# Kernel optimization log

Hardware: AMD Instinct MI355X
Metric: run time of the kernel (lower is better)

## Reference

```python
import jax, jax.numpy as jnp
import numpy as np


def _layernorm(x, g, b, eps=1e-5):
    m = x.mean(-1, keepdims=True)
    v = ((x - m) ** 2).mean(-1, keepdims=True)
    return (x - m) * jax.lax.rsqrt(v + eps) * g + b


def _rmsnorm(x, w, eps=1e-6):
    return x * jax.lax.rsqrt((x * x).mean(-1, keepdims=True) + eps) * w


def setup_inputs() -> dict:
    key = jax.random.key(0)
    ks = jax.random.split(key, 8)
    B, T, S, C_img = 1, 3, 880, 3072
    C_mouse, D_hid, Dd = 2, 1024, 64
    vin = C_img + 12 * C_mouse  # 3096 = img_hidden + mouse_dim_in*vae_tcr*windows
    w = lambda k, shp: (jax.random.normal(k, shp, jnp.float32) * 0.02)
    return dict(
        x=jax.random.normal(ks[0], (B, T * S, C_img), jnp.float32),
        condition=jax.random.normal(ks[1], (B, 12, C_mouse), jnp.float32),
        w1=w(ks[2], (vin, D_hid)), b1=jnp.zeros((D_hid,), jnp.float32),
        w2=w(ks[3], (D_hid, D_hid)), b2=jnp.zeros((D_hid,), jnp.float32),
        ln_g=jnp.ones((D_hid,), jnp.float32), ln_b=jnp.zeros((D_hid,), jnp.float32),
        wqkv=w(ks[4], (D_hid, 3 * D_hid)), bqkv=jnp.zeros((3 * D_hid,), jnp.float32),
        qn_w=jnp.ones((Dd,), jnp.float32), kn_w=jnp.ones((Dd,), jnp.float32),
        wproj=w(ks[5], (D_hid, C_img)), bproj=jnp.zeros((C_img,), jnp.float32),
        H=22, W=40, temporal_shape=3, num_frame_per_block=3,
    )


def reference(x, condition, w1, b1, w2, b2, ln_g, ln_b, wqkv, bqkv,
              qn_w, kn_w, wproj, bproj, H, W, temporal_shape, num_frame_per_block):
    B, T_S, C_img = x.shape
    T = temporal_shape
    if condition.shape[1] > 9:
        condition = condition[:, -12:, :]
    _, N_frames, C = condition.shape
    action_len, pad_len = 20, 12
    pad = jnp.zeros((B, action_len - N_frames, C), condition.dtype)
    mouse_padded = jnp.concatenate([pad, condition], axis=1)  # [B, 20, C]
    # windowed gather: fixed small loop over num_frame_per_block (<=3)
    wins = jnp.stack([mouse_padded[:, i * 4:i * 4 + pad_len, :]
                      for i in range(num_frame_per_block)], axis=1)  # [B, F, 12, C]
    gm = wins.reshape(B, num_frame_per_block, pad_len * C)  # [B, F, 12C]
    S = 880  # hardcoded in original forward
    gm = jnp.broadcast_to(gm[:, None], (B, S, num_frame_per_block, pad_len * C))
    gm = gm.reshape(B * S, num_frame_per_block, pad_len * C)
    # fuse broadcast mouse features with image tokens (raw row-major reshape, as in torch)
    fused = jnp.concatenate([x.reshape(B * S, T, C_img), gm], axis=-1)  # [BS, T, C_img+12C]
    h = jax.nn.gelu(fused @ w1 + b1, approximate=True) @ w2 + b2
    h = _layernorm(h, ln_g, ln_b)  # [BS, T, D_hid]
    qkv = h @ wqkv + bqkv  # [BS, T, 3*D_hid]
    Dd = qn_w.shape[0]
    Hh = qkv.shape[-1] // (3 * Dd)
    qkv = qkv.reshape(B * S, T, 3, Hh, Dd)
    q, k, v = qkv[:, :, 0], qkv[:, :, 1], qkv[:, :, 2]
    q = _rmsnorm(q, qn_w).astype(v.dtype)
    k = _rmsnorm(k, kn_w).astype(v.dtype)
    # original flattens to one sequence of BS*T tokens for single_prefill (non-causal)
    N = B * S * T
    qf = q.reshape(N, Hh, Dd)
    kf = k.reshape(N, Hh, Dd)
    vf = v.reshape(N, Hh, Dd)
    scale = 1.0 / np.sqrt(Dd).astype(np.float32)
    scores = jnp.einsum('nhd,mhd->hnm', qf, kf) * scale  # [Hh, N, N]
    attn = jax.nn.softmax(scores, axis=-1)
    o = jnp.einsum('hnm,mhd->nhd', attn, vf)  # [N, Hh, Dd]
    # '(B S) T H D -> B (T S) (H D)'
    o = o.reshape(B, S, T, Hh, Dd).transpose(0, 2, 1, 3, 4).reshape(B, T * S, Hh * Dd)
    out = o @ wproj + bproj
    return x + out
```

## Files before the change

kernel.cpp:

```cpp
#include <hip/hip_runtime.h>
#include <hip/hip_bf16.h>

typedef __attribute__((ext_vector_type(8))) short short8;
typedef __attribute__((ext_vector_type(4))) short short4v;
typedef __attribute__((ext_vector_type(4))) unsigned uint4v;
typedef __attribute__((ext_vector_type(4))) float f32x4;
typedef __attribute__((ext_vector_type(16))) float f32x16;
typedef unsigned short u16;

#define ZERO16 (f32x16){0,0,0,0,0,0,0,0,0,0,0,0,0,0,0,0}

__device__ __forceinline__ float b2f(u16 h) {
    unsigned u = ((unsigned)h) << 16;
    float f; __builtin_memcpy(&f, &u, 4); return f;
}
__device__ __forceinline__ u16 f2b(float f) {
    __hip_bfloat16 h = __float2bfloat16(f);
    u16 r; __builtin_memcpy(&r, &h, 2); return r;
}
__device__ __forceinline__ void gload16(const void* g, void* l) {
    __builtin_amdgcn_global_load_lds(
        (const __attribute__((address_space(1))) unsigned*)g,
        (__attribute__((address_space(3))) unsigned*)l, 16, 0, 0);
}
__device__ __forceinline__ unsigned cvtpk_bf16(float lo, float hi) {
    unsigned d;
    asm("v_cvt_pk_bf16_f32 %0, %1, %2" : "=v"(d) : "v"(lo), "v"(hi));
    return d;
}

#define M_VALID 2640
#define M_PAD   2688
#define K1      3096
#define K1P     3136
#define DH      1024
#define CIMG    3072
#define NHEAD   16
#define NT      84
#define QTP     42
#define NSPLIT  3
#define TILES_PER_SPLIT 28
#define LOG2E   1.4426950408889634f

__global__ __launch_bounds__(256) void build_fused_kernel(
    const float* __restrict__ x, const float* __restrict__ cond,
    u16* __restrict__ fused)
{
    int n = blockIdx.x;
    int tid = threadIdx.x;
    const float* xr = x + (size_t)n * CIMG;
    u16* fr = fused + (size_t)n * K1P;
    for (int c = tid * 4; c < CIMG; c += 1024) {
        float4 v = *(const float4*)(xr + c);
        short4v w;
        w[0] = (short)f2b(v.x); w[1] = (short)f2b(v.y);
        w[2] = (short)f2b(v.z); w[3] = (short)f2b(v.w);
        *(short4v*)(fr + c) = w;
    }
    if (tid < 16) {
        int t = n % 3;
        short4v w;
        for (int jj = 0; jj < 4; jj++) {
            int j = tid * 4 + jj;
            float val = 0.f;
            if (j < 24) {
                int f = t * 4 + (j >> 1);
                if (f >= 8) val = cond[(f - 8) * 2 + (j & 1)];
            }
            w[jj] = (short)f2b(val);
        }
        *(short4v*)(fr + CIMG + tid * 4) = w;
    }
}

__global__ __launch_bounds__(256) void transpose_all_kernel(
    const float* __restrict__ w1, const float* __restrict__ w2,
    const float* __restrict__ wqkv, const float* __restrict__ wproj,
    u16* __restrict__ w1t, u16* __restrict__ w2t,
    u16* __restrict__ wqkvt, u16* __restrict__ wprojt)
{
    int b = blockIdx.x;
    const float* W; u16* Wt; int K, N, ldt, nx;
    if (b < 3136)      {            W = w1;    Wt = w1t;    K = K1; N = DH;   ldt = K1P; nx = 32; }
    else if (b < 4160) { b -= 3136; W = w2;    Wt = w2t;    K = DH; N = DH;   ldt = DH;  nx = 32; }
    else if (b < 7232) { b -= 4160; W = wqkv;  Wt = wqkvt;  K = DH; N = 3072; ldt = DH;  nx = 96; }
    else               { b -= 7232; W = wproj; Wt = wprojt; K = DH; N = CIMG; ldt = DH;  nx = 96; }
    __shared__ float t[32][33];
    int n0 = (b % nx) * 32, k0 = (b / nx) * 32;
    int x = threadIdx.x & 31, y0 = threadIdx.x >> 5;
    for (int yy = y0; yy < 32; yy += 8) {
        int k = k0 + yy, n = n0 + x;
        t[yy][x] = (k < K && n < N) ? W[(size_t)k * N + n] : 0.f;
    }
    __syncthreads();
    for (int yy = y0; yy < 32; yy += 8) {
        int n = n0 + yy, k = k0 + x;
        if (n < N && k < ldt) Wt[(size_t)n * ldt + k] = f2b(t[x][yy]);
    }
}

template<int EPI, int BM, int BN>
__global__ __launch_bounds__(256) void gemm_kernel(
    const u16* __restrict__ A, const u16* __restrict__ Bt,
    const float* __restrict__ bias, const float* __restrict__ resid,
    u16* __restrict__ Cb, float* __restrict__ Cf,
    int N, int K, int Mvalid)
{
    constexpr int MI  = BM / 32;
    constexpr int NJ  = BN / 32;
    constexpr int CA  = BM / 32;
    constexpr int CB  = BN / 32;
    constexpr unsigned ABYTES = BM * 128;
    constexpr unsigned BBYTES = BN * 128;
    constexpr unsigned STG = 2 * (ABYTES + BBYTES);
    constexpr unsigned CTW = BN + 4;
    constexpr unsigned CTB = BM * CTW * 4;
    constexpr int TPR = 256 / BM;
    __shared__ __align__(16) char smem[STG > CTB ? STG : CTB];

    const int tid = threadIdx.x;
    const int lane = tid & 63, wid = tid >> 6;
    const int l15 = lane & 15, l4 = lane >> 4;

    const int nx = N / BN;
    const int nwg = nx * (M_PAD / BM);
    const int bid = blockIdx.x;
    const int wgid = (bid & 7) * (nwg >> 3) + (bid >> 3);
    const int m0 = (wgid / nx) * BM, n0 = (wgid % nx) * BN;

    const int wr = (wid >> 1) * (BM / 2), wc = (wid & 1) * (BN / 2);

    const int srow = lane >> 3;
    const int scol = ((lane & 7) ^ (lane >> 3)) << 3;

    f32x4 acc[MI][NJ];
#pragma unroll
    for (int i = 0; i < MI; i++)
#pragma unroll
        for (int j = 0; j < NJ; j++) acc[i][j] = (f32x4){0.f, 0.f, 0.f, 0.f};

    const int nt = K >> 6;

    auto stage = [&](int buf, int k0) {
        char* Ab = smem + buf * ABYTES;
        char* Bb = smem + 2 * ABYTES + buf * BBYTES;
#pragma unroll
        for (int i = 0; i < CA; i++) {
            int c = wid * CA + i;
            gload16(A + (size_t)(m0 + c * 8 + srow) * K + k0 + scol,
                    Ab + c * 1024 + lane * 16);
        }
#pragma unroll
        for (int i = 0; i < CB; i++) {
            int c = wid * CB + i;
            gload16(Bt + (size_t)(n0 + c * 8 + srow) * K + k0 + scol,
                    Bb + c * 1024 + lane * 16);
        }
    };

    stage(0, 0);
    __syncthreads();
    int cur = 0;
    for (int t = 0; t < nt; t++) {
        if (t + 1 < nt) stage(cur ^ 1, (t + 1) * 64);
        const char* Ab = smem + cur * ABYTES;
        const char* Bb = smem + 2 * ABYTES + cur * BBYTES;
#pragma unroll
        for (int ki = 0; ki < 2; ki++) {
            short8 af[MI], bfr[NJ];
#pragma unroll
            for (int i = 0; i < MI; i++) {
                int row = wr + i * 16 + l15;
                af[i] = *(const short8*)(Ab + row * 128 + (((ki * 4 + l4) ^ (l15 & 7)) << 4));
            }
#pragma unroll
            for (int j = 0; j < NJ; j++) {
                int row = wc + j * 16 + l15;
                bfr[j] = *(const short8*)(Bb + row * 128 + (((ki * 4 + l4) ^ (l15 & 7)) << 4));
            }
            __builtin_amdgcn_s_setprio(1);
#pragma unroll
            for (int i = 0; i < MI; i++)
#pragma unroll
                for (int j = 0; j < NJ; j++)
                    acc[i][j] = __builtin_amdgcn_mfma_f32_16x16x32_bf16(af[i], bfr[j], acc[i][j], 0, 0, 0);
            __builtin_amdgcn_s_setprio(0);
        }
        __syncthreads();
        cur ^= 1;
    }

    float* Ct = (float*)smem;
#pragma unroll
    for (int i = 0; i < MI; i++)
#pragma unroll
        for (int j = 0; j < NJ; j++)
#pragma unroll
            for (int r = 0; r < 4; r++)
                Ct[(wr + i * 16 + l4 * 4 + r) * CTW + wc + j * 16 + l15] = acc[i][j][r];
    __syncthreads();

    const int row = tid / TPR;
    const int cb  = (tid % TPR) * (BN / TPR);
    const int grow = m0 + row;
    const int gcol = n0 + cb;
    if (EPI == 2) {
        if (grow < Mvalid) {
#pragma unroll
            for (int u = 0; u < BN / (4 * TPR); u++) {
                f32x4 v = *(const f32x4*)&Ct[row * CTW + cb + u * 4];
                float4 bv = *(const float4*)&bias[gcol + u * 4];
                float4 rv = *(const float4*)&resid[(size_t)grow * N + gcol + u * 4];
                float4 o;
                o.x = v[0] + bv.x + rv.x; o.y = v[1] + bv.y + rv.y;
                o.z = v[2] + bv.z + rv.z; o.w = v[3] + bv.w + rv.w;
                *(float4*)&Cf[(size_t)grow * N + gcol + u * 4] = o;
            }
        }
    } else {
        u16 tmp[BN / TPR];
#pragma unroll
        for (int u = 0; u < BN / (4 * TPR); u++) {
            f32x4 v = *(const f32x4*)&Ct[row * CTW + cb + u * 4];
            float4 bv = *(const float4*)&bias[gcol + u * 4];
#pragma unroll
            for (int e = 0; e < 4; e++) {
                float val = v[e] + ((const float*)&bv)[e];
                if (EPI == 0) {
                    float tt = val + 0.044715f * val * val * val;
                    val = 0.5f * val * (1.0f + tanhf(0.7978845608028654f * tt));
                }
                tmp[u * 4 + e] = f2b(val);
            }
        }
#pragma unroll
        for (int u = 0; u < BN / (8 * TPR); u++)
            *(short8*)(Cb + (size_t)grow * N + gcol + u * 8) = *(const short8*)&tmp[u * 8];
    }
}

__global__ __launch_bounds__(256) void ln_kernel(
    const u16* __restrict__ h2, const float* __restrict__ g,
    const float* __restrict__ b, u16* __restrict__ out)
{
    int row = blockIdx.x;
    int tid = threadIdx.x;
    const u16* p = h2 + (size_t)row * DH;
    float v[4];
#pragma unroll
    for (int i = 0; i < 4; i++) v[i] = b2f(p[tid * 4 + i]);
    float s1 = v[0] + v[1] + v[2] + v[3];
    float s2 = v[0]*v[0] + v[1]*v[1] + v[2]*v[2] + v[3]*v[3];
    for (int m = 1; m < 64; m <<= 1) { s1 += __shfl_xor(s1, m); s2 += __shfl_xor(s2, m); }
    __shared__ float a1[4], a2[4];
    int w = tid >> 6;
    if ((tid & 63) == 0) { a1[w] = s1; a2[w] = s2; }
    __syncthreads();
    s1 = a1[0] + a1[1] + a1[2] + a1[3];
    s2 = a2[0] + a2[1] + a2[2] + a2[3];
    float mean = s1 * (1.0f / 1024.0f);
    float var = s2 * (1.0f / 1024.0f) - mean * mean;
    float rs = rsqrtf(var + 1e-5f);
    u16* q = out + (size_t)row * DH;
#pragma unroll
    for (int i = 0; i < 4; i++) {
        int c = tid * 4 + i;
        q[c] = f2b((v[i] - mean) * rs * g[c] + b[c]);
    }
}

__global__ __launch_bounds__(256) void fragmentize_kernel(
    const u16* __restrict__ qkv, const float* __restrict__ qw, const float* __restrict__ kw,
    u16* __restrict__ Qf, u16* __restrict__ Kf, u16* __restrict__ Vf)
{
    __shared__ u16 Vlds[8 * 32 * 80];
    const int kt = blockIdx.x;
    const int hg = blockIdx.y;
    const int tid = threadIdx.x;
    const int t32 = tid >> 3, c8 = tid & 7;
    const int n = kt * 32 + t32;
    const u16* row = qkv + (size_t)n * 3072;

#pragma unroll
    for (int hh = 0; hh < 8; hh++) {
        short8 v = *(const short8*)(row + 2048 + (hg * 8 + hh) * 64 + c8 * 8);
        *(short8*)(&Vlds[(hh * 32 + t32) * 80 + c8 * 8]) = v;
    }

    float sq[8], sk[8];
#pragma unroll
    for (int hh = 0; hh < 8; hh++) {
        int h = hg * 8 + hh;
        short8 qv = *(const short8*)(row + h * 64 + c8 * 8);
        short8 kv = *(const short8*)(row + 1024 + h * 64 + c8 * 8);
        float aq = 0.f, ak = 0.f;
#pragma unroll
        for (int e = 0; e < 8; e++) {
            float fq = b2f((u16)qv[e]); aq += fq * fq;
            float fk = b2f((u16)kv[e]); ak += fk * fk;
        }
        sq[hh] = aq; sk[hh] = ak;
    }
#pragma unroll
    for (int m = 1; m < 8; m <<= 1) {
#pragma unroll
        for (int hh = 0; hh < 8; hh++) {
            sq[hh] += __shfl_xor(sq[hh], m);
            sk[hh] += __shfl_xor(sk[hh], m);
        }
    }

    float qwv[8], kwv[8];
#pragma unroll
    for (int e = 0; e < 8; e++) { qwv[e] = qw[c8 * 8 + e]; kwv[e] = kw[c8 * 8 + e]; }

#pragma unroll
    for (int hh = 0; hh < 8; hh++) {
        int h = hg * 8 + hh;
        float rq = rsqrtf(sq[hh] * (1.0f / 64.0f) + 1e-6f) * (0.125f * LOG2E);
        float rk = rsqrtf(sk[hh] * (1.0f / 64.0f) + 1e-6f);
        short8 qv = *(const short8*)(row + h * 64 + c8 * 8);
        short8 kv = *(const short8*)(row + 1024 + h * 64 + c8 * 8);
        short8 qo, ko;
#pragma unroll
        for (int e = 0; e < 8; e++) {
            qo[e] = (short)f2b(b2f((u16)qv[e]) * rq * qwv[e]);
            ko[e] = (short)f2b(b2f((u16)kv[e]) * rk * kwv[e]);
        }
        size_t base = (((size_t)(h * NT + kt) * 4 + (c8 >> 1)) << 9) + t32 * 16 + (c8 & 1) * 8;
        *(short8*)(Qf + base) = qo;
        *(short8*)(Kf + base) = ko;
    }

    __syncthreads();

    const int fd = tid >> 6;
    const int lkq = (tid & 63) >> 1, lhi = tid & 1;
#pragma unroll
    for (int hh = 0; hh < 8; hh++) {
        int h = hg * 8 + hh;
        short8 o;
#pragma unroll
        for (int e = 0; e < 8; e++)
            o[e] = (short)Vlds[(hh * 32 + (fd & 1) * 16 + lhi * 8 + e) * 80 + (fd >> 1) * 32 + lkq];
        *(short8*)(Vf + (((size_t)(h * NT + kt) * 4 + fd) << 9) + lkq * 16 + lhi * 8) = o;
    }
}

__device__ __forceinline__ void attn_tile(
    f32x16& st, float& lr, f32x16& o0, f32x16& o1, const short8* vv)
{
    float sum = 0.f;
    float p[16];
#pragma unroll
    for (int r = 0; r < 16; r++) { p[r] = __builtin_amdgcn_exp2f(st[r]); sum += p[r]; }
    lr += sum + __shfl_xor(sum, 32);

    unsigned a0 = cvtpk_bf16(p[0], p[1]),   a1 = cvtpk_bf16(p[2], p[3]);
    unsigned a2 = cvtpk_bf16(p[4], p[5]),   a3 = cvtpk_bf16(p[6], p[7]);
    unsigned a4 = cvtpk_bf16(p[8], p[9]),   a5 = cvtpk_bf16(p[10], p[11]);
    unsigned a6 = cvtpk_bf16(p[12], p[13]), a7 = cvtpk_bf16(p[14], p[15]);
    asm("v_permlane32_swap_b32 %0, %1" : "+v"(a0), "+v"(a2));
    asm("v_permlane32_swap_b32 %0, %1" : "+v"(a1), "+v"(a3));
    asm("v_permlane32_swap_b32 %0, %1" : "+v"(a4), "+v"(a6));
    asm("v_permlane32_swap_b32 %0, %1" : "+v"(a5), "+v"(a7));
    uint4v u0 = {a0, a1, a2, a3}, u1 = {a4, a5, a6, a7};
    short8 pa0, pa1;
    __builtin_memcpy(&pa0, &u0, 16);
    __builtin_memcpy(&pa1, &u1, 16);

    __builtin_amdgcn_s_setprio(1);
    o0 = __builtin_amdgcn_mfma_f32_32x32x16_bf16(pa0, vv[0], o0, 0, 0, 0);
    o0 = __builtin_amdgcn_mfma_f32_32x32x16_bf16(pa1, vv[1], o0, 0, 0, 0);
    o1 = __builtin_amdgcn_mfma_f32_32x32x16_bf16(pa0, vv[2], o1, 0, 0, 0);
    o1 = __builtin_amdgcn_mfma_f32_32x32x16_bf16(pa1, vv[3], o1, 0, 0, 0);
    __builtin_amdgcn_s_setprio(0);
}

__global__ __launch_bounds__(128, 4) void attn_kernel(
    const u16* __restrict__ Qf, const u16* __restrict__ Kf,
    const u16* __restrict__ Vf, u16* __restrict__ part, float* __restrict__ ml)
{
    const int nwg = NSPLIT * NHEAD * QTP;
    const int bid = blockIdx.x;
    const int wgid = (bid & 7) * (nwg >> 3) + (bid >> 3);
    const int s   = wgid / (NHEAD * QTP);
    const int rem = wgid % (NHEAD * QTP);
    const int h   = rem / QTP;
    const int qtp = rem % QTP;
    const int wid = threadIdx.x >> 6;
    const int qt  = qtp * 2 + wid;
    const int lane = threadIdx.x & 63;
    const int kq = lane & 31;
    const int hi = lane >> 5;
    const int q0 = qt * 32;
    const int lxy = kq * 16 + hi * 8;
    const u16* Kh = Kf + ((size_t)h * NT * 4 << 9);
    const u16* Vh = Vf + ((size_t)h * NT * 4 << 9);

    short8 qf[4];
#pragma unroll
    for (int d = 0; d < 4; d++)
        qf[d] = *(const short8*)(Qf + (((size_t)(h * NT + qt) * 4 + d) << 9) + lxy);

    f32x16 o0 = ZERO16, o1 = ZERO16;
    float lr = 0.f;

    const int ts0 = s * TILES_PER_SPLIT;
    short8 kf[4];
#pragma unroll
    for (int d = 0; d < 4; d++)
        kf[d] = *(const short8*)(Kh + (((size_t)ts0 * 4 + d) << 9) + lxy);

    for (int i = 0; i < TILES_PER_SPLIT; i++) {
        const int tile = ts0 + i;
        const int k0 = tile * 32;
        short8 vv[4];
#pragma unroll
        for (int fd = 0; fd < 4; fd++)
            vv[fd] = *(const short8*)(Vh + (((size_t)tile * 4 + fd) << 9) + lxy);

        f32x16 st = ZERO16;
        __builtin_amdgcn_s_setprio(1);
#pragma unroll
        for (int d = 0; d < 4; d++)
            st = __builtin_amdgcn_mfma_f32_32x32x16_bf16(kf[d], qf[d], st, 0, 0, 0);
        __builtin_amdgcn_s_setprio(0);

        if (i < TILES_PER_SPLIT - 1) {
#pragma unroll
            for (int d = 0; d < 4; d++)
                kf[d] = *(const short8*)(Kh + (((size_t)(tile + 1) * 4 + d) << 9) + lxy);
        }

        if (k0 + 32 > M_VALID) {
#pragma unroll
            for (int r = 0; r < 16; r++) {
                int key = k0 + (r & 3) + 8 * (r >> 2) + 4 * hi;
                if (key >= M_VALID) st[r] = -3.0e38f;
            }
        }
        attn_tile(st, lr, o0, o1, vv);
    }

#pragma unroll
    for (int r = 0; r < 16; r++) {
        int rl = (r & 3) + 8 * (r >> 2) + 4 * hi;
        int qrow = q0 + rl;
        if (qrow < M_VALID) {
            u16* pp = part + ((size_t)s * M_PAD + qrow) * DH + h * 64;
            pp[kq] = f2b(o0[r]);
            pp[kq + 32] = f2b(o1[r]);
        }
    }
    if (hi == 0 && q0 + kq < M_VALID)
        ml[((size_t)s * NHEAD + h) * M_PAD + q0 + kq] = lr;
}

__global__ __launch_bounds__(256) void attn_merge_kernel(
    const u16* __restrict__ part, const float* __restrict__ ml, u16* __restrict__ obf)
{
    const int q = blockIdx.x;
    const int t = threadIdx.x;
    const int h = t >> 4, i = t & 15;
    float L = 0.f;
#pragma unroll
    for (int s = 0; s < NSPLIT; s++)
        L += ml[((size_t)s * NHEAD + h) * M_PAD + q];
    float inv = 1.0f / L;
    float4 acc = {0.f, 0.f, 0.f, 0.f};
#pragma unroll
    for (int s = 0; s < NSPLIT; s++) {
        short4v v = *(const short4v*)(part + ((size_t)s * M_PAD + q) * DH + h * 64 + i * 4);
        acc.x += b2f((u16)v[0]); acc.y += b2f((u16)v[1]);
        acc.z += b2f((u16)v[2]); acc.w += b2f((u16)v[3]);
    }
    int mrow = (q % 3) * 880 + q / 3;
    short4v w;
    w[0] = (short)f2b(acc.x * inv); w[1] = (short)f2b(acc.y * inv);
    w[2] = (short)f2b(acc.z * inv); w[3] = (short)f2b(acc.w * inv);
    *(short4v*)(obf + (size_t)mrow * DH + h * 64 + i * 4) = w;
}

extern "C" void kernel_launch(void* const* d_in, const int* in_sizes, int n_in,
                              void* d_out, int out_size, void* d_ws, size_t ws_size,
                              hipStream_t stream)
{
    const float* x      = (const float*)d_in[0];
    const float* cond   = (const float*)d_in[1];
    const float* w1     = (const float*)d_in[2];
    const float* b1     = (const float*)d_in[3];
    const float* w2     = (const float*)d_in[4];
    const float* b2     = (const float*)d_in[5];
    const float* ln_g   = (const float*)d_in[6];
    const float* ln_b   = (const float*)d_in[7];
    const float* wqkv   = (const float*)d_in[8];
    const float* bqkv   = (const float*)d_in[9];
    const float* qn_w   = (const float*)d_in[10];
    const float* kn_w   = (const float*)d_in[11];
    const float* wproj  = (const float*)d_in[12];
    const float* bproj  = (const float*)d_in[13];
    float* out = (float*)d_out;

    char* ws = (char*)d_ws;
    size_t off = 0;
    auto alloc = [&](size_t bytes) { size_t o = off; off += (bytes + 255) & ~(size_t)255; return o; };

    size_t off_fused  = alloc((size_t)M_PAD * K1P * 2);
    size_t off_w1t    = alloc((size_t)DH * K1P * 2);
    size_t off_w2t    = alloc((size_t)DH * DH * 2);
    size_t off_wqkvt  = alloc((size_t)3072 * DH * 2);
    size_t off_wprojt = alloc((size_t)CIMG * DH * 2);
    size_t off_h1     = alloc((size_t)M_PAD * DH * 2);
    size_t off_h2     = alloc((size_t)M_PAD * DH * 2);
    size_t off_h2ln   = alloc((size_t)M_PAD * DH * 2);
    size_t off_qkv    = alloc((size_t)M_PAD * 3072 * 2);
    size_t off_qf     = alloc((size_t)NHEAD * NT * 4 * 512 * 2);
    size_t off_kf     = alloc((size_t)NHEAD * NT * 4 * 512 * 2);
    size_t off_vf     = alloc((size_t)NHEAD * NT * 4 * 512 * 2);
    size_t off_obf    = alloc((size_t)M_PAD * DH * 2);
    (void)ws_size;

    u16* fused  = (u16*)(ws + off_fused);
    u16* w1t    = (u16*)(ws + off_w1t);
    u16* w2t    = (u16*)(ws + off_w2t);
    u16* wqkvt  = (u16*)(ws + off_wqkvt);
    u16* wprojt = (u16*)(ws + off_wprojt);
    u16* h1     = (u16*)(ws + off_h1);
    u16* h2     = (u16*)(ws + off_h2);
    u16* h2ln   = (u16*)(ws + off_h2ln);
    u16* qkvb   = (u16*)(ws + off_qkv);
    u16* Qf     = (u16*)(ws + off_qf);
    u16* Kf     = (u16*)(ws + off_kf);
    u16* Vf     = (u16*)(ws + off_vf);
    u16* obf    = (u16*)(ws + off_obf);
    u16* part   = (u16*)(ws + off_h1);
    float* mlbf = (float*)(ws + off_fused);

    hipMemsetAsync(ws + off_fused + (size_t)M_VALID * K1P * 2, 0, (size_t)(M_PAD - M_VALID) * K1P * 2, stream);

    build_fused_kernel<<<M_VALID, 256, 0, stream>>>(x, cond, fused);
    transpose_all_kernel<<<10304, 256, 0, stream>>>(w1, w2, wqkv, wproj, w1t, w2t, wqkvt, wprojt);

    gemm_kernel<0, 64, 64><<<dim3((DH / 64) * (M_PAD / 64)), 256, 0, stream>>>(fused, w1t, b1, nullptr, h1, nullptr, DH, K1P, M_PAD);
    gemm_kernel<1, 64, 64><<<dim3((DH / 64) * (M_PAD / 64)), 256, 0, stream>>>(h1, w2t, b2, nullptr, h2, nullptr, DH, DH, M_PAD);
    ln_kernel<<<M_PAD, 256, 0, stream>>>(h2, ln_g, ln_b, h2ln);
    gemm_kernel<1, 128, 128><<<dim3((3072 / 128) * (M_PAD / 128)), 256, 0, stream>>>(h2ln, wqkvt, bqkv, nullptr, qkvb, nullptr, 3072, DH, M_PAD);
    fragmentize_kernel<<<dim3(NT, 2), 256, 0, stream>>>(qkvb, qn_w, kn_w, Qf, Kf, Vf);
    attn_kernel<<<dim3(NSPLIT * NHEAD * QTP), 128, 0, stream>>>(Qf, Kf, Vf, part, mlbf);
    attn_merge_kernel<<<M_VALID, 256, 0, stream>>>(part, mlbf, obf);
    gemm_kernel<2, 128, 128><<<dim3((CIMG / 128) * (M_PAD / 128)), 256, 0, stream>>>(obf, wprojt, bproj, x, nullptr, out, CIMG, DH, M_VALID);
}
```

Measured before the change: 188.6 us.

## Fold mouse-condition columns into per-frame bias and double-buffer attention K tiles

The 24 broadcast mouse-condition columns of the first GEMM input are replaced by a precomputed per-frame bias (b1 plus cond times the matching w1 rows), indexed by row mod 3. This shrinks the first GEMM's K dimension from 3136 to 3072 and removes the pad memset and the extra fused-column writes. Separately, the attention loop now computes QK^T for two key tiles at a time with double-buffered K loads and moves the V loads into the softmax/PV helper. The attention kernel's occupancy hint drops from 4 to 2 blocks to allow more registers. With the memset gone, the padded rows of the fused buffer are left uninitialized, which could let non-finite values reach masked attention rows.

```diff
diff --git a/kernel.cpp b/kernel.cpp
--- a/kernel.cpp
+++ b/kernel.cpp
@@ -31,8 +31,7 @@
 
 #define M_VALID 2640
 #define M_PAD   2688
-#define K1      3096
-#define K1P     3136
+#define K1P     3072
 #define DH      1024
 #define CIMG    3072
 #define NHEAD   16
@@ -43,8 +42,7 @@
 #define LOG2E   1.4426950408889634f
 
 __global__ __launch_bounds__(256) void build_fused_kernel(
-    const float* __restrict__ x, const float* __restrict__ cond,
-    u16* __restrict__ fused)
+    const float* __restrict__ x, u16* __restrict__ fused)
 {
     int n = blockIdx.x;
     int tid = threadIdx.x;
@@ -57,20 +55,21 @@
         w[2] = (short)f2b(v.z); w[3] = (short)f2b(v.w);
         *(short4v*)(fr + c) = w;
     }
-    if (tid < 16) {
-        int t = n % 3;
-        short4v w;
-        for (int jj = 0; jj < 4; jj++) {
-            int j = tid * 4 + jj;
-            float val = 0.f;
-            if (j < 24) {
-                int f = t * 4 + (j >> 1);
-                if (f >= 8) val = cond[(f - 8) * 2 + (j & 1)];
-            }
-            w[jj] = (short)f2b(val);
-        }
-        *(short4v*)(fr + CIMG + tid * 4) = w;
-    }
+}
+
+__global__ __launch_bounds__(256) void bias1t_kernel(
+    const float* __restrict__ w1, const float* __restrict__ b1,
+    const float* __restrict__ cond, float* __restrict__ bias1t)
+{
+    int t = blockIdx.x;
+    int col = blockIdx.y * 256 + threadIdx.x;
+    float v = b1[col];
+#pragma unroll
+    for (int j = 0; j < 24; j++) {
+        int f = t * 4 + (j >> 1);
+        if (f >= 8) v += cond[(f - 8) * 2 + (j & 1)] * w1[(size_t)(3072 + j) * DH + col];
+    }
+    bias1t[t * DH + col] = v;
 }
 
 __global__ __launch_bounds__(256) void transpose_all_kernel(
@@ -81,10 +80,10 @@
 {
     int b = blockIdx.x;
     const float* W; u16* Wt; int K, N, ldt, nx;
-    if (b < 3136)      {            W = w1;    Wt = w1t;    K = K1; N = DH;   ldt = K1P; nx = 32; }
-    else if (b < 4160) { b -= 3136; W = w2;    Wt = w2t;    K = DH; N = DH;   ldt = DH;  nx = 32; }
-    else if (b < 7232) { b -= 4160; W = wqkv;  Wt = wqkvt;  K = DH; N = 3072; ldt = DH;  nx = 96; }
-    else               { b -= 7232; W = wproj; Wt = wprojt; K = DH; N = CIMG; ldt = DH;  nx = 96; }
+    if (b < 3072)      {            W = w1;    Wt = w1t;    K = 3072; N = DH;   ldt = 3072; nx = 32; }
+    else if (b < 4096) { b -= 3072; W = w2;    Wt = w2t;    K = DH;   N = DH;   ldt = DH;   nx = 32; }
+    else if (b < 7168) { b -= 4096; W = wqkv;  Wt = wqkvt;  K = DH;   N = 3072; ldt = DH;   nx = 96; }
+    else               { b -= 7168; W = wproj; Wt = wprojt; K = DH;   N = CIMG; ldt = DH;   nx = 96; }
     __shared__ float t[32][33];
     int n0 = (b % nx) * 32, k0 = (b / nx) * 32;
     int x = threadIdx.x & 31, y0 = threadIdx.x >> 5;
@@ -218,11 +217,12 @@
             }
         }
     } else {
+        const float* bb = bias + (EPI == 0 ? (size_t)(grow % 3) * N : 0);
         u16 tmp[BN / TPR];
 #pragma unroll
         for (int u = 0; u < BN / (4 * TPR); u++) {
             f32x4 v = *(const f32x4*)&Ct[row * CTW + cb + u * 4];
-            float4 bv = *(const float4*)&bias[gcol + u * 4];
+            float4 bv = *(const float4*)&bb[gcol + u * 4];
 #pragma unroll
             for (int e = 0; e < 4; e++) {
                 float val = v[e] + ((const float*)&bv)[e];
@@ -348,12 +348,22 @@
 }
 
 __device__ __forceinline__ void attn_tile(
-    f32x16& st, float& lr, f32x16& o0, f32x16& o1, const short8* vv)
-{
-    float sum = 0.f;
+    f32x16& st, float& lr, f32x16& o0, f32x16& o1,
+    const u16* __restrict__ Vh, int tile, int lxy)
+{
+    short8 vv[4];
+#pragma unroll
+    for (int fd = 0; fd < 4; fd++)
+        vv[fd] = *(const short8*)(Vh + (((size_t)tile * 4 + fd) << 9) + lxy);
+
     float p[16];
 #pragma unroll
-    for (int r = 0; r < 16; r++) { p[r] = __builtin_amdgcn_exp2f(st[r]); sum += p[r]; }
+    for (int r = 0; r < 16; r++) p[r] = __builtin_amdgcn_exp2f(st[r]);
+    float s0 = (p[0] + p[1]) + (p[2] + p[3]);
+    float s1 = (p[4] + p[5]) + (p[6] + p[7]);
+    float s2 = (p[8] + p[9]) + (p[10] + p[11]);
+    float s3 = (p[12] + p[13]) + (p[14] + p[15]);
+    float sum = (s0 + s1) + (s2 + s3);
     lr += sum + __shfl_xor(sum, 32);
 
     unsigned a0 = cvtpk_bf16(p[0], p[1]),   a1 = cvtpk_bf16(p[2], p[3]);
@@ -377,7 +387,7 @@
     __builtin_amdgcn_s_setprio(0);
 }
 
-__global__ __launch_bounds__(128, 4) void attn_kernel(
+__global__ __launch_bounds__(128, 2) void attn_kernel(
     const u16* __restrict__ Qf, const u16* __restrict__ Kf,
     const u16* __restrict__ Vf, u16* __restrict__ part, float* __restrict__ ml)
 {
@@ -405,34 +415,24 @@
 
     f32x16 o0 = ZERO16, o1 = ZERO16;
     float lr = 0.f;
-
     const int ts0 = s * TILES_PER_SPLIT;
-    short8 kf[4];
-#pragma unroll
-    for (int d = 0; d < 4; d++)
-        kf[d] = *(const short8*)(Kh + (((size_t)ts0 * 4 + d) << 9) + lxy);
-
-    for (int i = 0; i < TILES_PER_SPLIT; i++) {
-        const int tile = ts0 + i;
-        const int k0 = tile * 32;
-        short8 vv[4];
-#pragma unroll
-        for (int fd = 0; fd < 4; fd++)
-            vv[fd] = *(const short8*)(Vh + (((size_t)tile * 4 + fd) << 9) + lxy);
-
+
+    auto loadK = [&](short8* k, int tile) {
+#pragma unroll
+        for (int d = 0; d < 4; d++)
+            k[d] = *(const short8*)(Kh + (((size_t)tile * 4 + d) << 9) + lxy);
+    };
+    auto qk = [&](const short8* k) {
         f32x16 st = ZERO16;
         __builtin_amdgcn_s_setprio(1);
 #pragma unroll
         for (int d = 0; d < 4; d++)
-            st = __builtin_amdgcn_mfma_f32_32x32x16_bf16(kf[d], qf[d], st, 0, 0, 0);
+            st = __builtin_amdgcn_mfma_f32_32x32x16_bf16(k[d], qf[d], st, 0, 0, 0);
         __builtin_amdgcn_s_setprio(0);
-
-        if (i < TILES_PER_SPLIT - 1) {
-#pragma unroll
-            for (int d = 0; d < 4; d++)
-                kf[d] = *(const short8*)(Kh + (((size_t)(tile + 1) * 4 + d) << 9) + lxy);
-        }
-
+        return st;
+    };
+    auto mask = [&](f32x16& st, int tile) {
+        const int k0 = tile * 32;
         if (k0 + 32 > M_VALID) {
 #pragma unroll
             for (int r = 0; r < 16; r++) {
@@ -440,7 +440,21 @@
                 if (key >= M_VALID) st[r] = -3.0e38f;
             }
         }
-        attn_tile(st, lr, o0, o1, vv);
+    };
+
+    short8 kfA[4], kfB[4];
+    loadK(kfA, ts0);
+    loadK(kfB, ts0 + 1);
+
+    for (int i = 0; i < TILES_PER_SPLIT; i += 2) {
+        const int t0 = ts0 + i, t1 = t0 + 1;
+        f32x16 st0 = qk(kfA);
+        f32x16 st1 = qk(kfB);
+        if (i + 2 < TILES_PER_SPLIT) { loadK(kfA, t0 + 2); loadK(kfB, t0 + 3); }
+        mask(st0, t0);
+        attn_tile(st0, lr, o0, o1, Vh, t0, lxy);
+        mask(st1, t1);
+        attn_tile(st1, lr, o0, o1, Vh, t1, lxy);
     }
 
 #pragma unroll
@@ -519,6 +533,7 @@
     size_t off_kf     = alloc((size_t)NHEAD * NT * 4 * 512 * 2);
     size_t off_vf     = alloc((size_t)NHEAD * NT * 4 * 512 * 2);
     size_t off_obf    = alloc((size_t)M_PAD * DH * 2);
+    size_t off_b1t    = alloc((size_t)3 * DH * 4);
     (void)ws_size;
 
     u16* fused  = (u16*)(ws + off_fused);
@@ -534,15 +549,15 @@
     u16* Kf     = (u16*)(ws + off_kf);
     u16* Vf     = (u16*)(ws + off_vf);
     u16* obf    = (u16*)(ws + off_obf);
+    float* b1t  = (float*)(ws + off_b1t);
     u16* part   = (u16*)(ws + off_h1);
     float* mlbf = (float*)(ws + off_fused);
 
-    hipMemsetAsync(ws + off_fused + (size_t)M_VALID * K1P * 2, 0, (size_t)(M_PAD - M_VALID) * K1P * 2, stream);
-
-    build_fused_kernel<<<M_VALID, 256, 0, stream>>>(x, cond, fused);
-    transpose_all_kernel<<<10304, 256, 0, stream>>>(w1, w2, wqkv, wproj, w1t, w2t, wqkvt, wprojt);
-
-    gemm_kernel<0, 64, 64><<<dim3((DH / 64) * (M_PAD / 64)), 256, 0, stream>>>(fused, w1t, b1, nullptr, h1, nullptr, DH, K1P, M_PAD);
+    build_fused_kernel<<<M_VALID, 256, 0, stream>>>(x, fused);
+    bias1t_kernel<<<dim3(3, 4), 256, 0, stream>>>(w1, b1, cond, b1t);
+    transpose_all_kernel<<<10240, 256, 0, stream>>>(w1, w2, wqkv, wproj, w1t, w2t, wqkvt, wprojt);
+
+    gemm_kernel<0, 64, 64><<<dim3((DH / 64) * (M_PAD / 64)), 256, 0, stream>>>(fused, w1t, b1t, nullptr, h1, nullptr, DH, K1P, M_PAD);
     gemm_kernel<1, 64, 64><<<dim3((DH / 64) * (M_PAD / 64)), 256, 0, stream>>>(h1, w2t, b2, nullptr, h2, nullptr, DH, DH, M_PAD);
     ln_kernel<<<M_PAD, 256, 0, stream>>>(h2, ln_g, ln_b, h2ln);
     gemm_kernel<1, 128, 128><<<dim3((3072 / 128) * (M_PAD / 128)), 256, 0, stream>>>(h2ln, wqkvt, bqkv, nullptr, qkvb, nullptr, 3072, DH, M_PAD);
```

Measured after the change: 192.0 us. No clear change (+1.8%).
